# Optimization experiments

Measured on AMD Instinct MI355X. Metric: run time of the kernel, lower is better.

Reference implementation:

```python
import jax, jax.numpy as jnp
import numpy as np


def setup_inputs() -> dict:
    key = jax.random.key(0)
    k1, k2, *kw = jax.random.split(key, 12)
    N, E = 10000, 320000
    D_IN, D_HID, D_EMB, D_PRED = 2, 128, 256, 128

    def lin(k, fan_in, fan_out):
        bound = 1.0 / np.sqrt(fan_in)
        kw_, kb_ = jax.random.split(k)
        W = jax.random.uniform(kw_, (fan_in, fan_out), jnp.float32, -bound, bound)
        b = jax.random.uniform(kb_, (fan_out,), jnp.float32, -bound, bound)
        return W, b

    W1, b1 = lin(kw[0], D_IN, D_HID)
    W2, b2 = lin(kw[1], D_HID, D_EMB)
    Wp1, bp1 = lin(kw[2], D_EMB, D_PRED)
    Wp2, bp2 = lin(kw[3], D_PRED, 1)

    src = jax.random.randint(k1, (E,), 0, N, dtype=jnp.int32)
    dst = jax.random.randint(k2, (E,), 0, N, dtype=jnp.int32)
    return {
        "W1": W1, "b1": b1, "W2": W2, "b2": b2,
        "Wp1": Wp1, "bp1": bp1, "Wp2": Wp2, "bp2": bp2,
        "src": src, "dst": dst, "num_nodes": N,
    }


def reference(W1, b1, W2, b2, Wp1, bp1, Wp2, bp2, src, dst, num_nodes):
    N = num_nodes
    E = src.shape[0]
    ones = jnp.ones((E,), jnp.float32)
    # node features = [in_degree, out_degree]  -> [N, 2]
    in_deg = jax.ops.segment_sum(ones, dst, num_segments=N)
    out_deg = jax.ops.segment_sum(ones, src, num_segments=N)
    x = jnp.stack([in_deg, out_deg], axis=1)

    def gcn_agg(h):
        # sum of messages from source nodes into destination nodes (SpMM-like)
        return jax.ops.segment_sum(h[src], dst, num_segments=N)

    h = jax.nn.relu(gcn_agg(x) @ W1 + b1)        # [N, 128]
    h = gcn_agg(h) @ W2 + b2                     # [N, 256]
    h = jax.nn.relu(h)
    graph_embedding = jnp.sum(h, axis=0)         # [256] (dgl.sum_nodes, single graph)
    m = jax.nn.relu(graph_embedding @ Wp1 + bp1)
    metric = m @ Wp2 + bp2                       # [1]
    return (graph_embedding, metric)
```

## Files before the change

kernel.cpp:

```cpp
#include <hip/hip_runtime.h>

#define N_NODES 10000
#define CAPLOG 7
#define CAP 128
#define NPART 16
#define NBH 128
#define TBH 512

__global__ __launch_bounds__(TBH) void hist_kernel(const int* __restrict__ src,
                                                   const int* __restrict__ dst,
                                                   unsigned int* __restrict__ cnt,
                                                   float* __restrict__ ge_p,
                                                   unsigned int* __restrict__ done,
                                                   int E) {
  __shared__ unsigned int hist[N_NODES];
  const int tid = threadIdx.x, bid = blockIdx.x;
  for (int i = tid; i < N_NODES; i += TBH) hist[i] = 0;
  if (bid < NPART && tid < 256) ge_p[(bid << 8) + tid] = 0.f;
  if (bid == NPART && tid == 0) *done = 0u;
  __syncthreads();
  const int chunk = (E + NBH - 1) / NBH;
  const int e0 = bid * chunk, e1 = min(E, e0 + chunk);
  for (int e = e0 + tid; e < e1; e += TBH) {
    atomicAdd(&hist[dst[e]], 1u);
    atomicAdd(&hist[src[e]], 0x10000u);
  }
  __syncthreads();
  unsigned int* outb = cnt + (size_t)bid * N_NODES;
  for (int i = tid; i < N_NODES; i += TBH) outb[i] = hist[i];
}

__global__ __launch_bounds__(256) void scan_kernel(const unsigned int* __restrict__ cnt,
                                                   unsigned int* __restrict__ off,
                                                   unsigned int* __restrict__ pack) {
  const int n = blockIdx.x * 256 + threadIdx.x;
  if (n >= N_NODES) return;
  unsigned run = 0;
#pragma unroll 8
  for (int b = 0; b < NBH; ++b) {
    unsigned v = cnt[(size_t)b * N_NODES + n];
    off[(size_t)b * N_NODES + n] = run;
    run += v;
  }
  pack[n] = run;
}

__global__ __launch_bounds__(TBH) void scatter_kernel(const int* __restrict__ src,
                                                      const int* __restrict__ dst,
                                                      const unsigned int* __restrict__ off,
                                                      unsigned short* __restrict__ slots,
                                                      int E) {
  __shared__ unsigned int cur[N_NODES];
  const int tid = threadIdx.x, bid = blockIdx.x;
  const unsigned int* ob = off + (size_t)bid * N_NODES;
  for (int i = tid; i < N_NODES; i += TBH) cur[i] = ob[i];
  __syncthreads();
  const int chunk = (E + NBH - 1) / NBH;
  const int e0 = bid * chunk, e1 = min(E, e0 + chunk);
  for (int e = e0 + tid; e < e1; e += TBH) {
    int d = dst[e];
    unsigned idx = atomicAdd(&cur[d], 1u) & 0xFFFFu;
    if (idx < CAP) slots[(d << CAPLOG) + idx] = (unsigned short)src[e];
  }
}

__global__ __launch_bounds__(256) void agg1_kernel(const unsigned int* __restrict__ pack,
                                                   const unsigned short* __restrict__ slots,
                                                   unsigned int* __restrict__ a) {
  const int tid = threadIdx.x;
  const int hw = tid >> 5, hl = tid & 31;
  const int node = blockIdx.x * 8 + hw;
  const int deg = min((int)(pack[node] & 0xFFFFu), CAP);
  const int base = node << CAPLOG;
  unsigned acc = 0u;
  for (int e = hl; e < deg; e += 32) acc += pack[slots[base + e]];
#pragma unroll
  for (int off = 16; off > 0; off >>= 1) acc += (unsigned)__shfl_xor((int)acc, off, 32);
  if (hl == 0) a[node] = acc;
}

__global__ __launch_bounds__(256) void agg2gemm2_kernel(const unsigned int* __restrict__ pack,
                                                        const unsigned short* __restrict__ slots,
                                                        const unsigned int* __restrict__ a,
                                                        const float* __restrict__ W1,
                                                        const float* __restrict__ b1,
                                                        const float* __restrict__ W2,
                                                        const float* __restrict__ b2,
                                                        const float* __restrict__ Wp1,
                                                        const float* __restrict__ bp1,
                                                        const float* __restrict__ Wp2,
                                                        const float* __restrict__ bp2,
                                                        float* __restrict__ ge_p,
                                                        unsigned int* __restrict__ done,
                                                        float* __restrict__ out) {
  __shared__ float2 s_a[8][CAP + 1];
  __shared__ float s_tile[8][128];
  __shared__ float s_ge[256];
  __shared__ float s_m[256];
  __shared__ int s_last;
  const int tid = threadIdx.x, bid = blockIdx.x;
  const int hw = tid >> 5, hl = tid & 31;

  const int node = bid * 8 + hw;
  const int deg = min((int)(pack[node] & 0xFFFFu), CAP);
  const int base = node << CAPLOG;
  for (int e = hl; e < deg; e += 32) {
    const unsigned v = a[slots[base + e]];
    s_a[hw][e] = make_float2((float)(v & 0xFFFFu), (float)(v >> 16));
  }

  float w10[4], w11[4], bb[4];
#pragma unroll
  for (int c = 0; c < 4; ++c) {
    w10[c] = W1[4 * hl + c];
    w11[c] = W1[128 + 4 * hl + c];
    bb[c] = b1[4 * hl + c];
  }
  __syncthreads();

  float acc0 = 0.f, acc1 = 0.f, acc2 = 0.f, acc3 = 0.f;
#pragma unroll 4
  for (int j = 0; j < deg; ++j) {
    const float2 av = s_a[hw][j];
    acc0 += fmaxf(fmaf(av.x, w10[0], fmaf(av.y, w11[0], bb[0])), 0.f);
    acc1 += fmaxf(fmaf(av.x, w10[1], fmaf(av.y, w11[1], bb[1])), 0.f);
    acc2 += fmaxf(fmaf(av.x, w10[2], fmaf(av.y, w11[2], bb[2])), 0.f);
    acc3 += fmaxf(fmaf(av.x, w10[3], fmaf(av.y, w11[3], bb[3])), 0.f);
  }
  s_tile[hw][4 * hl + 0] = acc0;
  s_tile[hw][4 * hl + 1] = acc1;
  s_tile[hw][4 * hl + 2] = acc2;
  s_tile[hw][4 * hl + 3] = acc3;
  __syncthreads();

  float d[8];
#pragma unroll
  for (int n = 0; n < 8; ++n) d[n] = 0.f;
#pragma unroll
  for (int kc = 0; kc < 4; ++kc) {
    float wv[32];
#pragma unroll
    for (int c = 0; c < 32; ++c) wv[c] = W2[(kc * 32 + c) * 256 + tid];
#pragma unroll
    for (int n = 0; n < 8; ++n) {
      const float4* row4 = (const float4*)&s_tile[n][kc * 32];
      float t0 = 0.f, t1 = 0.f, t2 = 0.f, t3 = 0.f;
#pragma unroll
      for (int q = 0; q < 8; ++q) {
        float4 rv = row4[q];
        t0 = fmaf(rv.x, wv[4 * q + 0], t0);
        t1 = fmaf(rv.y, wv[4 * q + 1], t1);
        t2 = fmaf(rv.z, wv[4 * q + 2], t2);
        t3 = fmaf(rv.w, wv[4 * q + 3], t3);
      }
      d[n] += (t0 + t1) + (t2 + t3);
    }
  }

  const float bj = b2[tid];
  float accge = 0.f;
#pragma unroll
  for (int n = 0; n < 8; ++n) accge += fmaxf(d[n] + bj, 0.f);
  atomicAdd(&ge_p[((bid & (NPART - 1)) << 8) + tid], accge);

  __syncthreads();
  if (tid == 0) {
    __threadfence();
    s_last = (atomicAdd(done, 1u) == (unsigned)(gridDim.x - 1)) ? 1 : 0;
  }
  __syncthreads();
  if (!s_last) return;

  float g = 0.f;
#pragma unroll
  for (int p = 0; p < NPART; ++p)
    g += __hip_atomic_load(&ge_p[p * 256 + tid], __ATOMIC_RELAXED, __HIP_MEMORY_SCOPE_AGENT);
  s_ge[tid] = g;
  out[tid] = g;
  __syncthreads();
  const int j = tid & 127, halfk = tid >> 7;
  float dd = halfk ? 0.f : bp1[j];
  const int k0 = halfk << 7;
#pragma unroll 8
  for (int k = k0; k < k0 + 128; ++k) dd = fmaf(s_ge[k], Wp1[k * 128 + j], dd);
  s_m[tid] = dd;
  __syncthreads();
  if (tid < 128) s_m[tid] = fmaxf(s_m[tid] + s_m[tid + 128], 0.f) * Wp2[tid];
  __syncthreads();
  if (tid < 64) {
    float v = s_m[tid] + s_m[tid + 64];
#pragma unroll
    for (int off = 32; off > 0; off >>= 1) v += __shfl_xor(v, off);
    if (tid == 0) out[256] = v + bp2[0];
  }
}

extern "C" void kernel_launch(void* const* d_in, const int* in_sizes, int n_in,
                              void* d_out, int out_size, void* d_ws, size_t ws_size,
                              hipStream_t stream) {
  const float* W1 = (const float*)d_in[0];
  const float* b1 = (const float*)d_in[1];
  const float* W2 = (const float*)d_in[2];
  const float* b2 = (const float*)d_in[3];
  const float* Wp1 = (const float*)d_in[4];
  const float* bp1 = (const float*)d_in[5];
  const float* Wp2 = (const float*)d_in[6];
  const float* bp2 = (const float*)d_in[7];
  const int* src = (const int*)d_in[8];
  const int* dst = (const int*)d_in[9];
  const int E = in_sizes[8];
  const int N = N_NODES;

  char* p = (char*)d_ws;
  float* ge_p = (float*)p;               p += (size_t)NPART * 256 * 4;
  unsigned int* done = (unsigned int*)p; p += 16;
  unsigned int* pack = (unsigned int*)p; p += (size_t)N * 4;
  unsigned int* a = (unsigned int*)p;    p += (size_t)N * 4;
  unsigned short* slots = (unsigned short*)p; p += (size_t)N * CAP * 2;
  unsigned int* cnt = (unsigned int*)p;  p += (size_t)NBH * N * 4;
  unsigned int* off = (unsigned int*)p;
  float* out = (float*)d_out;

  hist_kernel<<<NBH, TBH, 0, stream>>>(src, dst, cnt, ge_p, done, E);
  scan_kernel<<<(N + 255) / 256, 256, 0, stream>>>(cnt, off, pack);
  scatter_kernel<<<NBH, TBH, 0, stream>>>(src, dst, off, slots, E);
  agg1_kernel<<<N / 8, 256, 0, stream>>>(pack, slots, a);
  agg2gemm2_kernel<<<N / 8, 256, 0, stream>>>(pack, slots, a, W1, b1, W2, b2,
                                              Wp1, bp1, Wp2, bp2, ge_p, done, out);
}
```

Before: 145.4 us.

## Replace histogram/scan/scatter with global-atomic slot fill and widen gemm tile

Drops the three-kernel private-histogram, prefix-scan and scatter build of the adjacency slots in favour of one memset plus a single kernel. That kernel uses global atomics on an interleaved in/out degree counter to claim slots and count degrees. This avoids writing and reading the 128xN count and offset arrays and two launches, at the cost of contended global atomics. Separately, the fused agg2/gemm kernel now handles 16 nodes per block instead of 8, so each W2 load is reused across more rows, with higher register pressure.

```diff
diff --git a/kernel.cpp b/kernel.cpp
--- a/kernel.cpp
+++ b/kernel.cpp
@@ -4,82 +4,55 @@
 #define CAPLOG 7
 #define CAP 128
 #define NPART 16
-#define NBH 128
-#define TBH 512
-
-__global__ __launch_bounds__(TBH) void hist_kernel(const int* __restrict__ src,
-                                                   const int* __restrict__ dst,
-                                                   unsigned int* __restrict__ cnt,
-                                                   float* __restrict__ ge_p,
-                                                   unsigned int* __restrict__ done,
-                                                   int E) {
-  __shared__ unsigned int hist[N_NODES];
-  const int tid = threadIdx.x, bid = blockIdx.x;
-  for (int i = tid; i < N_NODES; i += TBH) hist[i] = 0;
-  if (bid < NPART && tid < 256) ge_p[(bid << 8) + tid] = 0.f;
-  if (bid == NPART && tid == 0) *done = 0u;
-  __syncthreads();
-  const int chunk = (E + NBH - 1) / NBH;
-  const int e0 = bid * chunk, e1 = min(E, e0 + chunk);
-  for (int e = e0 + tid; e < e1; e += TBH) {
-    atomicAdd(&hist[dst[e]], 1u);
-    atomicAdd(&hist[src[e]], 0x10000u);
-  }
-  __syncthreads();
-  unsigned int* outb = cnt + (size_t)bid * N_NODES;
-  for (int i = tid; i < N_NODES; i += TBH) outb[i] = hist[i];
-}
-
-__global__ __launch_bounds__(256) void scan_kernel(const unsigned int* __restrict__ cnt,
-                                                   unsigned int* __restrict__ off,
-                                                   unsigned int* __restrict__ pack) {
-  const int n = blockIdx.x * 256 + threadIdx.x;
-  if (n >= N_NODES) return;
-  unsigned run = 0;
-#pragma unroll 8
-  for (int b = 0; b < NBH; ++b) {
-    unsigned v = cnt[(size_t)b * N_NODES + n];
-    off[(size_t)b * N_NODES + n] = run;
-    run += v;
-  }
-  pack[n] = run;
-}
-
-__global__ __launch_bounds__(TBH) void scatter_kernel(const int* __restrict__ src,
+
+#define TSC 256
+__global__ __launch_bounds__(TSC) void scatter_atomic(const int* __restrict__ src,
                                                       const int* __restrict__ dst,
-                                                      const unsigned int* __restrict__ off,
+                                                      unsigned int* __restrict__ cur2,
                                                       unsigned short* __restrict__ slots,
                                                       int E) {
-  __shared__ unsigned int cur[N_NODES];
-  const int tid = threadIdx.x, bid = blockIdx.x;
-  const unsigned int* ob = off + (size_t)bid * N_NODES;
-  for (int i = tid; i < N_NODES; i += TBH) cur[i] = ob[i];
-  __syncthreads();
-  const int chunk = (E + NBH - 1) / NBH;
-  const int e0 = bid * chunk, e1 = min(E, e0 + chunk);
-  for (int e = e0 + tid; e < e1; e += TBH) {
-    int d = dst[e];
-    unsigned idx = atomicAdd(&cur[d], 1u) & 0xFFFFu;
-    if (idx < CAP) slots[(d << CAPLOG) + idx] = (unsigned short)src[e];
-  }
-}
-
-__global__ __launch_bounds__(256) void agg1_kernel(const unsigned int* __restrict__ pack,
+  const int t = blockIdx.x * TSC + threadIdx.x;
+  const int nv = E >> 2;
+  if (t < nv) {
+    const int4 s4 = ((const int4*)src)[t];
+    const int4 d4 = ((const int4*)dst)[t];
+    const int ss[4] = {s4.x, s4.y, s4.z, s4.w};
+    const int dd[4] = {d4.x, d4.y, d4.z, d4.w};
+#pragma unroll
+    for (int q = 0; q < 4; ++q) {
+      const unsigned idx = atomicAdd(&cur2[dd[q] << 1], 1u);
+      if (idx < CAP) slots[(dd[q] << CAPLOG) + idx] = (unsigned short)ss[q];
+      atomicAdd(&cur2[(ss[q] << 1) + 1], 1u);
+    }
+  }
+  if (t == 0) {
+    for (int e = E & ~3; e < E; ++e) {
+      const unsigned idx = atomicAdd(&cur2[dst[e] << 1], 1u);
+      if (idx < CAP) slots[(dst[e] << CAPLOG) + idx] = (unsigned short)src[e];
+      atomicAdd(&cur2[(src[e] << 1) + 1], 1u);
+    }
+  }
+}
+
+__global__ __launch_bounds__(256) void agg1_kernel(const unsigned int* __restrict__ cur2,
                                                    const unsigned short* __restrict__ slots,
                                                    unsigned int* __restrict__ a) {
   const int tid = threadIdx.x;
   const int hw = tid >> 5, hl = tid & 31;
   const int node = blockIdx.x * 8 + hw;
-  const int deg = min((int)(pack[node] & 0xFFFFu), CAP);
+  const int deg = min((int)cur2[node << 1], CAP);
   const int base = node << CAPLOG;
   unsigned acc = 0u;
-  for (int e = hl; e < deg; e += 32) acc += pack[slots[base + e]];
+  for (int e = hl; e < deg; e += 32) {
+    const uint2 c = ((const uint2*)cur2)[slots[base + e]];
+    acc += c.x | (c.y << 16);
+  }
 #pragma unroll
   for (int off = 16; off > 0; off >>= 1) acc += (unsigned)__shfl_xor((int)acc, off, 32);
   if (hl == 0) a[node] = acc;
 }
 
-__global__ __launch_bounds__(256) void agg2gemm2_kernel(const unsigned int* __restrict__ pack,
+__global__ __launch_bounds__(256) void agg2gemm2_kernel(const unsigned int* __restrict__ cur2,
                                                         const unsigned short* __restrict__ slots,
                                                         const unsigned int* __restrict__ a,
                                                         const float* __restrict__ W1,
@@ -93,20 +66,23 @@
                                                         float* __restrict__ ge_p,
                                                         unsigned int* __restrict__ done,
                                                         float* __restrict__ out) {
-  __shared__ float2 s_a[8][CAP + 1];
-  __shared__ float s_tile[8][128];
+  __shared__ float2 s_a[16][CAP + 1];
+  __shared__ float s_tile[16][128];
   __shared__ float s_ge[256];
   __shared__ float s_m[256];
   __shared__ int s_last;
   const int tid = threadIdx.x, bid = blockIdx.x;
   const int hw = tid >> 5, hl = tid & 31;
 
-  const int node = bid * 8 + hw;
-  const int deg = min((int)(pack[node] & 0xFFFFu), CAP);
-  const int base = node << CAPLOG;
-  for (int e = hl; e < deg; e += 32) {
-    const unsigned v = a[slots[base + e]];
-    s_a[hw][e] = make_float2((float)(v & 0xFFFFu), (float)(v >> 16));
+#pragma unroll
+  for (int nn = 0; nn < 2; ++nn) {
+    const int node = bid * 16 + hw * 2 + nn;
+    const int deg = min((int)cur2[node << 1], CAP);
+    const int base = node << CAPLOG;
+    for (int e = hl; e < deg; e += 32) {
+      const unsigned v = a[slots[base + e]];
+      s_a[hw * 2 + nn][e] = make_float2((float)(v & 0xFFFFu), (float)(v >> 16));
+    }
   }
 
   float w10[4], w11[4], bb[4];
@@ -118,31 +94,36 @@
   }
   __syncthreads();
 
-  float acc0 = 0.f, acc1 = 0.f, acc2 = 0.f, acc3 = 0.f;
+#pragma unroll
+  for (int nn = 0; nn < 2; ++nn) {
+    const int row = hw * 2 + nn;
+    const int node = bid * 16 + row;
+    const int deg = min((int)cur2[node << 1], CAP);
+    float acc0 = 0.f, acc1 = 0.f, acc2 = 0.f, acc3 = 0.f;
 #pragma unroll 4
-  for (int j = 0; j < deg; ++j) {
-    const float2 av = s_a[hw][j];
-    acc0 += fmaxf(fmaf(av.x, w10[0], fmaf(av.y, w11[0], bb[0])), 0.f);
-    acc1 += fmaxf(fmaf(av.x, w10[1], fmaf(av.y, w11[1], bb[1])), 0.f);
-    acc2 += fmaxf(fmaf(av.x, w10[2], fmaf(av.y, w11[2], bb[2])), 0.f);
-    acc3 += fmaxf(fmaf(av.x, w10[3], fmaf(av.y, w11[3], bb[3])), 0.f);
-  }
-  s_tile[hw][4 * hl + 0] = acc0;
-  s_tile[hw][4 * hl + 1] = acc1;
-  s_tile[hw][4 * hl + 2] = acc2;
-  s_tile[hw][4 * hl + 3] = acc3;
-  __syncthreads();
-
-  float d[8];
-#pragma unroll
-  for (int n = 0; n < 8; ++n) d[n] = 0.f;
-#pragma unroll
+    for (int j = 0; j < deg; ++j) {
+      const float2 av = s_a[row][j];
+      acc0 += fmaxf(fmaf(av.x, w10[0], fmaf(av.y, w11[0], bb[0])), 0.f);
+      acc1 += fmaxf(fmaf(av.x, w10[1], fmaf(av.y, w11[1], bb[1])), 0.f);
+      acc2 += fmaxf(fmaf(av.x, w10[2], fmaf(av.y, w11[2], bb[2])), 0.f);
+      acc3 += fmaxf(fmaf(av.x, w10[3], fmaf(av.y, w11[3], bb[3])), 0.f);
+    }
+    s_tile[row][4 * hl + 0] = acc0;
+    s_tile[row][4 * hl + 1] = acc1;
+    s_tile[row][4 * hl + 2] = acc2;
+    s_tile[row][4 * hl + 3] = acc3;
+  }
+  __syncthreads();
+
+  float d[16];
+#pragma unroll
+  for (int n = 0; n < 16; ++n) d[n] = 0.f;
   for (int kc = 0; kc < 4; ++kc) {
     float wv[32];
 #pragma unroll
     for (int c = 0; c < 32; ++c) wv[c] = W2[(kc * 32 + c) * 256 + tid];
 #pragma unroll
-    for (int n = 0; n < 8; ++n) {
+    for (int n = 0; n < 16; ++n) {
       const float4* row4 = (const float4*)&s_tile[n][kc * 32];
       float t0 = 0.f, t1 = 0.f, t2 = 0.f, t3 = 0.f;
 #pragma unroll
@@ -160,7 +141,7 @@
   const float bj = b2[tid];
   float accge = 0.f;
 #pragma unroll
-  for (int n = 0; n < 8; ++n) accge += fmaxf(d[n] + bj, 0.f);
+  for (int n = 0; n < 16; ++n) accge += fmaxf(d[n] + bj, 0.f);
   atomicAdd(&ge_p[((bid & (NPART - 1)) << 8) + tid], accge);
 
   __syncthreads();
@@ -209,22 +190,20 @@
   const int* src = (const int*)d_in[8];
   const int* dst = (const int*)d_in[9];
   const int E = in_sizes[8];
-  const int N = N_NODES;
 
   char* p = (char*)d_ws;
-  float* ge_p = (float*)p;               p += (size_t)NPART * 256 * 4;
-  unsigned int* done = (unsigned int*)p; p += 16;
-  unsigned int* pack = (unsigned int*)p; p += (size_t)N * 4;
-  unsigned int* a = (unsigned int*)p;    p += (size_t)N * 4;
-  unsigned short* slots = (unsigned short*)p; p += (size_t)N * CAP * 2;
-  unsigned int* cnt = (unsigned int*)p;  p += (size_t)NBH * N * 4;
-  unsigned int* off = (unsigned int*)p;
+  float* ge_p = (float*)p;               p += 16384;
+  unsigned int* cur2 = (unsigned int*)p; p += 80128;
+  unsigned int* done = (unsigned int*)p; p += 128;
+  unsigned short* slots = (unsigned short*)p; p += (size_t)N_NODES * CAP * 2;
+  unsigned int* a = (unsigned int*)p;
   float* out = (float*)d_out;
 
-  hist_kernel<<<NBH, TBH, 0, stream>>>(src, dst, cnt, ge_p, done, E);
-  scan_kernel<<<(N + 255) / 256, 256, 0, stream>>>(cnt, off, pack);
-  scatter_kernel<<<NBH, TBH, 0, stream>>>(src, dst, off, slots, E);
-  agg1_kernel<<<N / 8, 256, 0, stream>>>(pack, slots, a);
-  agg2gemm2_kernel<<<N / 8, 256, 0, stream>>>(pack, slots, a, W1, b1, W2, b2,
-                                              Wp1, bp1, Wp2, bp2, ge_p, done, out);
-}
+  hipMemsetAsync(d_ws, 0, 16384 + 80128 + 128, stream);
+
+  const int nv4 = (E + 3) / 4;
+  scatter_atomic<<<(nv4 + TSC - 1) / TSC, TSC, 0, stream>>>(src, dst, cur2, slots, E);
+  agg1_kernel<<<N_NODES / 8, 256, 0, stream>>>(cur2, slots, a);
+  agg2gemm2_kernel<<<N_NODES / 16, 256, 0, stream>>>(cur2, slots, a, W1, b1, W2, b2,
+                                                     Wp1, bp1, Wp2, bp2, ge_p, done, out);
+}
```

New measurement: 152.8 us. 5.1% more time.

## Split fused aggregation+GEMM kernel into separate aggregation and GEMM kernels

Applied to the files above, without the earlier changes.

Splits the fused second-layer aggregation and W2 GEMM kernel into two kernels. The first writes the aggregated 128-wide hidden rows to a new global buffer T, and the second reads T from global memory to do the GEMM, ReLU and graph-sum reduction. The intent is to stop the irregular, degree-dependent aggregation from stalling the GEMM work in the same block. The cost is an extra kernel launch and about 5 MB of global write and read traffic, with the GEMM now issuing scalar global loads instead of shared-memory float4 reads.

```diff
diff --git a/kernel.cpp b/kernel.cpp
--- a/kernel.cpp
+++ b/kernel.cpp
@@ -79,25 +79,13 @@
   if (hl == 0) a[node] = acc;
 }
 
-__global__ __launch_bounds__(256) void agg2gemm2_kernel(const unsigned int* __restrict__ pack,
-                                                        const unsigned short* __restrict__ slots,
-                                                        const unsigned int* __restrict__ a,
-                                                        const float* __restrict__ W1,
-                                                        const float* __restrict__ b1,
-                                                        const float* __restrict__ W2,
-                                                        const float* __restrict__ b2,
-                                                        const float* __restrict__ Wp1,
-                                                        const float* __restrict__ bp1,
-                                                        const float* __restrict__ Wp2,
-                                                        const float* __restrict__ bp2,
-                                                        float* __restrict__ ge_p,
-                                                        unsigned int* __restrict__ done,
-                                                        float* __restrict__ out) {
+__global__ __launch_bounds__(256) void aggT_kernel(const unsigned int* __restrict__ pack,
+                                                   const unsigned short* __restrict__ slots,
+                                                   const unsigned int* __restrict__ a,
+                                                   const float* __restrict__ W1,
+                                                   const float* __restrict__ b1,
+                                                   float* __restrict__ T) {
   __shared__ float2 s_a[8][CAP + 1];
-  __shared__ float s_tile[8][128];
-  __shared__ float s_ge[256];
-  __shared__ float s_m[256];
-  __shared__ int s_last;
   const int tid = threadIdx.x, bid = blockIdx.x;
   const int hw = tid >> 5, hl = tid & 31;
 
@@ -127,31 +115,46 @@
     acc2 += fmaxf(fmaf(av.x, w10[2], fmaf(av.y, w11[2], bb[2])), 0.f);
     acc3 += fmaxf(fmaf(av.x, w10[3], fmaf(av.y, w11[3], bb[3])), 0.f);
   }
-  s_tile[hw][4 * hl + 0] = acc0;
-  s_tile[hw][4 * hl + 1] = acc1;
-  s_tile[hw][4 * hl + 2] = acc2;
-  s_tile[hw][4 * hl + 3] = acc3;
-  __syncthreads();
-
-  float d[8];
-#pragma unroll
-  for (int n = 0; n < 8; ++n) d[n] = 0.f;
+  float4 tv;
+  tv.x = acc0; tv.y = acc1; tv.z = acc2; tv.w = acc3;
+  ((float4*)(T + (size_t)node * 128))[hl] = tv;
+}
+
+#define GNPB 8
+__global__ __launch_bounds__(256) void gemm2_kernel(const float* __restrict__ T,
+                                                    const float* __restrict__ W2,
+                                                    const float* __restrict__ b2,
+                                                    const float* __restrict__ Wp1,
+                                                    const float* __restrict__ bp1,
+                                                    const float* __restrict__ Wp2,
+                                                    const float* __restrict__ bp2,
+                                                    float* __restrict__ ge_p,
+                                                    unsigned int* __restrict__ done,
+                                                    float* __restrict__ out) {
+  __shared__ float s_ge[256];
+  __shared__ float s_m[256];
+  __shared__ int s_last;
+  const int tid = threadIdx.x, bid = blockIdx.x;
+  const int nbase = bid * GNPB;
+
+  float d[GNPB];
+#pragma unroll
+  for (int n = 0; n < GNPB; ++n) d[n] = 0.f;
 #pragma unroll
   for (int kc = 0; kc < 4; ++kc) {
     float wv[32];
 #pragma unroll
     for (int c = 0; c < 32; ++c) wv[c] = W2[(kc * 32 + c) * 256 + tid];
 #pragma unroll
-    for (int n = 0; n < 8; ++n) {
-      const float4* row4 = (const float4*)&s_tile[n][kc * 32];
+    for (int n = 0; n < GNPB; ++n) {
+      const float* trow = T + (size_t)(nbase + n) * 128 + kc * 32;
       float t0 = 0.f, t1 = 0.f, t2 = 0.f, t3 = 0.f;
 #pragma unroll
       for (int q = 0; q < 8; ++q) {
-        float4 rv = row4[q];
-        t0 = fmaf(rv.x, wv[4 * q + 0], t0);
-        t1 = fmaf(rv.y, wv[4 * q + 1], t1);
-        t2 = fmaf(rv.z, wv[4 * q + 2], t2);
-        t3 = fmaf(rv.w, wv[4 * q + 3], t3);
+        t0 = fmaf(trow[4 * q + 0], wv[4 * q + 0], t0);
+        t1 = fmaf(trow[4 * q + 1], wv[4 * q + 1], t1);
+        t2 = fmaf(trow[4 * q + 2], wv[4 * q + 2], t2);
+        t3 = fmaf(trow[4 * q + 3], wv[4 * q + 3], t3);
       }
       d[n] += (t0 + t1) + (t2 + t3);
     }
@@ -160,7 +163,7 @@
   const float bj = b2[tid];
   float accge = 0.f;
 #pragma unroll
-  for (int n = 0; n < 8; ++n) accge += fmaxf(d[n] + bj, 0.f);
+  for (int n = 0; n < GNPB; ++n) accge += fmaxf(d[n] + bj, 0.f);
   atomicAdd(&ge_p[((bid & (NPART - 1)) << 8) + tid], accge);
 
   __syncthreads();
@@ -217,6 +220,7 @@
   unsigned int* pack = (unsigned int*)p; p += (size_t)N * 4;
   unsigned int* a = (unsigned int*)p;    p += (size_t)N * 4;
   unsigned short* slots = (unsigned short*)p; p += (size_t)N * CAP * 2;
+  float* T = (float*)p;                  p += (size_t)N * 128 * 4;
   unsigned int* cnt = (unsigned int*)p;  p += (size_t)NBH * N * 4;
   unsigned int* off = (unsigned int*)p;
   float* out = (float*)d_out;
@@ -225,6 +229,7 @@
   scan_kernel<<<(N + 255) / 256, 256, 0, stream>>>(cnt, off, pack);
   scatter_kernel<<<NBH, TBH, 0, stream>>>(src, dst, off, slots, E);
   agg1_kernel<<<N / 8, 256, 0, stream>>>(pack, slots, a);
-  agg2gemm2_kernel<<<N / 8, 256, 0, stream>>>(pack, slots, a, W1, b1, W2, b2,
-                                              Wp1, bp1, Wp2, bp2, ge_p, done, out);
-}
+  aggT_kernel<<<N / 8, 256, 0, stream>>>(pack, slots, a, W1, b1, T);
+  gemm2_kernel<<<N / GNPB, 256, 0, stream>>>(T, W2, b2, Wp1, bp1, Wp2, bp2,
+                                             ge_p, done, out);
+}
```

Result: slower. 163.1 us (+12.2%).

## Register-tile layer-2 GEMM 4x4 per thread and process 16 nodes per block

Applied to the files above, without the earlier changes.

The fused aggregation+GEMM kernel now handles 16 nodes per block instead of 8, halving the grid. Each thread computes a 4-node by 4-column output tile, using float4 loads of W2 and of a padded shared tile. This replaces the old per-thread full-column scheme, which reloaded W2 rows per block, and adds a shared-memory reduction across node groups before the atomic. The intent is to cut W2 global traffic per node and improve FMA-to-load ratio. The cost is more shared memory, higher register pressure, and fewer blocks in flight.

```diff
diff --git a/kernel.cpp b/kernel.cpp
--- a/kernel.cpp
+++ b/kernel.cpp
@@ -6,6 +6,7 @@
 #define NPART 16
 #define NBH 128
 #define TBH 512
+#define TSTRIDE 132
 
 __global__ __launch_bounds__(TBH) void hist_kernel(const int* __restrict__ src,
                                                    const int* __restrict__ dst,
@@ -79,34 +80,49 @@
   if (hl == 0) a[node] = acc;
 }
 
-__global__ __launch_bounds__(256) void agg2gemm2_kernel(const unsigned int* __restrict__ pack,
-                                                        const unsigned short* __restrict__ slots,
-                                                        const unsigned int* __restrict__ a,
-                                                        const float* __restrict__ W1,
-                                                        const float* __restrict__ b1,
-                                                        const float* __restrict__ W2,
-                                                        const float* __restrict__ b2,
-                                                        const float* __restrict__ Wp1,
-                                                        const float* __restrict__ bp1,
-                                                        const float* __restrict__ Wp2,
-                                                        const float* __restrict__ bp2,
-                                                        float* __restrict__ ge_p,
-                                                        unsigned int* __restrict__ done,
-                                                        float* __restrict__ out) {
-  __shared__ float2 s_a[8][CAP + 1];
-  __shared__ float s_tile[8][128];
+#define FMA_ROW(aR0, aR1, aR2, aR3, t)                                       \
+  aR0 = fmaf(t.x, w0.x, aR0); aR0 = fmaf(t.y, w1.x, aR0);                    \
+  aR0 = fmaf(t.z, w2v.x, aR0); aR0 = fmaf(t.w, w3.x, aR0);                   \
+  aR1 = fmaf(t.x, w0.y, aR1); aR1 = fmaf(t.y, w1.y, aR1);                    \
+  aR1 = fmaf(t.z, w2v.y, aR1); aR1 = fmaf(t.w, w3.y, aR1);                   \
+  aR2 = fmaf(t.x, w0.z, aR2); aR2 = fmaf(t.y, w1.z, aR2);                    \
+  aR2 = fmaf(t.z, w2v.z, aR2); aR2 = fmaf(t.w, w3.z, aR2);                   \
+  aR3 = fmaf(t.x, w0.w, aR3); aR3 = fmaf(t.y, w1.w, aR3);                    \
+  aR3 = fmaf(t.z, w2v.w, aR3); aR3 = fmaf(t.w, w3.w, aR3);
+
+__global__ __launch_bounds__(256, 4) void agg2gemm2_kernel(const unsigned int* __restrict__ pack,
+                                                           const unsigned short* __restrict__ slots,
+                                                           const unsigned int* __restrict__ a,
+                                                           const float* __restrict__ W1,
+                                                           const float* __restrict__ b1,
+                                                           const float* __restrict__ W2,
+                                                           const float* __restrict__ b2,
+                                                           const float* __restrict__ Wp1,
+                                                           const float* __restrict__ bp1,
+                                                           const float* __restrict__ Wp2,
+                                                           const float* __restrict__ bp2,
+                                                           float* __restrict__ ge_p,
+                                                           unsigned int* __restrict__ done,
+                                                           float* __restrict__ out) {
+  __shared__ float2 s_a[16][CAP + 1];
+  __shared__ float s_t[16 * TSTRIDE];
+  __shared__ float s_red[4][256];
   __shared__ float s_ge[256];
   __shared__ float s_m[256];
   __shared__ int s_last;
   const int tid = threadIdx.x, bid = blockIdx.x;
   const int hw = tid >> 5, hl = tid & 31;
 
-  const int node = bid * 8 + hw;
-  const int deg = min((int)(pack[node] & 0xFFFFu), CAP);
-  const int base = node << CAPLOG;
-  for (int e = hl; e < deg; e += 32) {
-    const unsigned v = a[slots[base + e]];
-    s_a[hw][e] = make_float2((float)(v & 0xFFFFu), (float)(v >> 16));
+#pragma unroll
+  for (int nn = 0; nn < 2; ++nn) {
+    const int row = hw * 2 + nn;
+    const int node = bid * 16 + row;
+    const int deg = min((int)(pack[node] & 0xFFFFu), CAP);
+    const int base = node << CAPLOG;
+    for (int e = hl; e < deg; e += 32) {
+      const unsigned v = a[slots[base + e]];
+      s_a[row][e] = make_float2((float)(v & 0xFFFFu), (float)(v >> 16));
+    }
   }
 
   float w10[4], w11[4], bb[4];
@@ -118,50 +134,62 @@
   }
   __syncthreads();
 
-  float acc0 = 0.f, acc1 = 0.f, acc2 = 0.f, acc3 = 0.f;
+#pragma unroll
+  for (int nn = 0; nn < 2; ++nn) {
+    const int row = hw * 2 + nn;
+    const int node = bid * 16 + row;
+    const int deg = min((int)(pack[node] & 0xFFFFu), CAP);
+    float acc0 = 0.f, acc1 = 0.f, acc2 = 0.f, acc3 = 0.f;
 #pragma unroll 4
-  for (int j = 0; j < deg; ++j) {
-    const float2 av = s_a[hw][j];
-    acc0 += fmaxf(fmaf(av.x, w10[0], fmaf(av.y, w11[0], bb[0])), 0.f);
-    acc1 += fmaxf(fmaf(av.x, w10[1], fmaf(av.y, w11[1], bb[1])), 0.f);
-    acc2 += fmaxf(fmaf(av.x, w10[2], fmaf(av.y, w11[2], bb[2])), 0.f);
-    acc3 += fmaxf(fmaf(av.x, w10[3], fmaf(av.y, w11[3], bb[3])), 0.f);
-  }
-  s_tile[hw][4 * hl + 0] = acc0;
-  s_tile[hw][4 * hl + 1] = acc1;
-  s_tile[hw][4 * hl + 2] = acc2;
-  s_tile[hw][4 * hl + 3] = acc3;
-  __syncthreads();
-
-  float d[8];
-#pragma unroll
-  for (int n = 0; n < 8; ++n) d[n] = 0.f;
-#pragma unroll
-  for (int kc = 0; kc < 4; ++kc) {
-    float wv[32];
-#pragma unroll
-    for (int c = 0; c < 32; ++c) wv[c] = W2[(kc * 32 + c) * 256 + tid];
-#pragma unroll
-    for (int n = 0; n < 8; ++n) {
-      const float4* row4 = (const float4*)&s_tile[n][kc * 32];
-      float t0 = 0.f, t1 = 0.f, t2 = 0.f, t3 = 0.f;
-#pragma unroll
-      for (int q = 0; q < 8; ++q) {
-        float4 rv = row4[q];
-        t0 = fmaf(rv.x, wv[4 * q + 0], t0);
-        t1 = fmaf(rv.y, wv[4 * q + 1], t1);
-        t2 = fmaf(rv.z, wv[4 * q + 2], t2);
-        t3 = fmaf(rv.w, wv[4 * q + 3], t3);
-      }
-      d[n] += (t0 + t1) + (t2 + t3);
+    for (int j = 0; j < deg; ++j) {
+      const float2 av = s_a[row][j];
+      acc0 += fmaxf(fmaf(av.x, w10[0], fmaf(av.y, w11[0], bb[0])), 0.f);
+      acc1 += fmaxf(fmaf(av.x, w10[1], fmaf(av.y, w11[1], bb[1])), 0.f);
+      acc2 += fmaxf(fmaf(av.x, w10[2], fmaf(av.y, w11[2], bb[2])), 0.f);
+      acc3 += fmaxf(fmaf(av.x, w10[3], fmaf(av.y, w11[3], bb[3])), 0.f);
     }
-  }
-
-  const float bj = b2[tid];
-  float accge = 0.f;
-#pragma unroll
-  for (int n = 0; n < 8; ++n) accge += fmaxf(d[n] + bj, 0.f);
-  atomicAdd(&ge_p[((bid & (NPART - 1)) << 8) + tid], accge);
+    float* tr = s_t + row * TSTRIDE + 4 * hl;
+    tr[0] = acc0; tr[1] = acc1; tr[2] = acc2; tr[3] = acc3;
+  }
+  __syncthreads();
+
+  const int jq = tid & 63, ng = tid >> 6;
+  const int j = jq << 2;
+  const float* tb = s_t + (ng << 2) * TSTRIDE;
+  float a00 = 0.f, a01 = 0.f, a02 = 0.f, a03 = 0.f;
+  float a10 = 0.f, a11 = 0.f, a12 = 0.f, a13 = 0.f;
+  float a20 = 0.f, a21 = 0.f, a22 = 0.f, a23 = 0.f;
+  float a30 = 0.f, a31 = 0.f, a32 = 0.f, a33 = 0.f;
+#pragma unroll 4
+  for (int k = 0; k < 128; k += 4) {
+    const float4 w0 = *(const float4*)(W2 + (k + 0) * 256 + j);
+    const float4 w1 = *(const float4*)(W2 + (k + 1) * 256 + j);
+    const float4 w2v = *(const float4*)(W2 + (k + 2) * 256 + j);
+    const float4 w3 = *(const float4*)(W2 + (k + 3) * 256 + j);
+    const float4 t0 = *(const float4*)(tb + 0 * TSTRIDE + k);
+    const float4 t1 = *(const float4*)(tb + 1 * TSTRIDE + k);
+    const float4 t2 = *(const float4*)(tb + 2 * TSTRIDE + k);
+    const float4 t3 = *(const float4*)(tb + 3 * TSTRIDE + k);
+    FMA_ROW(a00, a01, a02, a03, t0)
+    FMA_ROW(a10, a11, a12, a13, t1)
+    FMA_ROW(a20, a21, a22, a23, t2)
+    FMA_ROW(a30, a31, a32, a33, t3)
+  }
+
+  const float4 bj = *(const float4*)(b2 + j);
+  float4 part;
+  part.x = fmaxf(a00 + bj.x, 0.f) + fmaxf(a10 + bj.x, 0.f) +
+           fmaxf(a20 + bj.x, 0.f) + fmaxf(a30 + bj.x, 0.f);
+  part.y = fmaxf(a01 + bj.y, 0.f) + fmaxf(a11 + bj.y, 0.f) +
+           fmaxf(a21 + bj.y, 0.f) + fmaxf(a31 + bj.y, 0.f);
+  part.z = fmaxf(a02 + bj.z, 0.f) + fmaxf(a12 + bj.z, 0.f) +
+           fmaxf(a22 + bj.z, 0.f) + fmaxf(a32 + bj.z, 0.f);
+  part.w = fmaxf(a03 + bj.w, 0.f) + fmaxf(a13 + bj.w, 0.f) +
+           fmaxf(a23 + bj.w, 0.f) + fmaxf(a33 + bj.w, 0.f);
+  *(float4*)(&s_red[ng][j]) = part;
+  __syncthreads();
+  const float g = (s_red[0][tid] + s_red[1][tid]) + (s_red[2][tid] + s_red[3][tid]);
+  atomicAdd(&ge_p[((bid & (NPART - 1)) << 8) + tid], g);
 
   __syncthreads();
   if (tid == 0) {
@@ -171,18 +199,18 @@
   __syncthreads();
   if (!s_last) return;
 
-  float g = 0.f;
+  float gg = 0.f;
 #pragma unroll
   for (int p = 0; p < NPART; ++p)
-    g += __hip_atomic_load(&ge_p[p * 256 + tid], __ATOMIC_RELAXED, __HIP_MEMORY_SCOPE_AGENT);
-  s_ge[tid] = g;
-  out[tid] = g;
-  __syncthreads();
-  const int j = tid & 127, halfk = tid >> 7;
-  float dd = halfk ? 0.f : bp1[j];
+    gg += __hip_atomic_load(&ge_p[p * 256 + tid], __ATOMIC_RELAXED, __HIP_MEMORY_SCOPE_AGENT);
+  s_ge[tid] = gg;
+  out[tid] = gg;
+  __syncthreads();
+  const int jh = tid & 127, halfk = tid >> 7;
+  float dd = halfk ? 0.f : bp1[jh];
   const int k0 = halfk << 7;
 #pragma unroll 8
-  for (int k = k0; k < k0 + 128; ++k) dd = fmaf(s_ge[k], Wp1[k * 128 + j], dd);
+  for (int k = k0; k < k0 + 128; ++k) dd = fmaf(s_ge[k], Wp1[k * 128 + jh], dd);
   s_m[tid] = dd;
   __syncthreads();
   if (tid < 128) s_m[tid] = fmaxf(s_m[tid] + s_m[tid + 128], 0.f) * Wp2[tid];
@@ -225,6 +253,6 @@
   scan_kernel<<<(N + 255) / 256, 256, 0, stream>>>(cnt, off, pack);
   scatter_kernel<<<NBH, TBH, 0, stream>>>(src, dst, off, slots, E);
   agg1_kernel<<<N / 8, 256, 0, stream>>>(pack, slots, a);
-  agg2gemm2_kernel<<<N / 8, 256, 0, stream>>>(pack, slots, a, W1, b1, W2, b2,
-                                              Wp1, bp1, Wp2, bp2, ge_p, done, out);
-}
+  agg2gemm2_kernel<<<N / 16, 256, 0, stream>>>(pack, slots, a, W1, b1, W2, b2,
+                                               Wp1, bp1, Wp2, bp2, ge_p, done, out);
+}
```

Measured after the change: 139.0 us. 4.4% less time.
